# Performance work log

Hardware: AMD Instinct MI355X
Metric: run time of the kernel (lower is better)

## Reference

```python
import jax, jax.numpy as jnp
import numpy as np

B, H, S, D = 4, 16, 2048, 64
TEMPERATURE = 8.0  # sqrt(D)
NEG = -1000000000.0

def setup_inputs() -> dict:
    key = jax.random.key(0)
    kq, kk, kv, km = jax.random.split(key, 4)
    q = jax.random.normal(kq, (B, H, S, D), dtype=jnp.float32)
    k = jax.random.normal(kk, (B, H, S, D), dtype=jnp.float32)
    v = jax.random.normal(kv, (B, H, S, D), dtype=jnp.float32)
    mask = jax.random.randint(km, (B, 1, S, S), 0, 2, dtype=jnp.int32)
    return {"q": q, "k": k, "v": v, "mask": mask}

def reference(q, k, v, mask):
    # scores: [B,H,S,S]
    scores = jnp.einsum('bhqd,bhkd->bhqk', q / TEMPERATURE, k)
    scores = jnp.where(mask == 1, NEG, scores)
    attn = jax.nn.softmax(scores, axis=-1)  # dropout p=0.0 -> identity
    out = jnp.einsum('bhqk,bhkd->bhqd', attn, v)
    return out
```

## Files before the change

kernel.cpp:

```cpp
#include <hip/hip_runtime.h>

#define NB 4
#define NH 16
#define SS 2048
#define DD 64
#define QT 128
#define KT 64
#define LSP 72
#define QSCALE 0.18033688011112042f

#define MASK_BITS_BYTES ((size_t)NB * SS * (SS / 8))
#define KV_TILE_ELEMS   (KT * DD)
#define KV_BYTES        ((size_t)NB * NH * SS * DD * 2)
#define WS_NEED         (MASK_BITS_BYTES + 2 * KV_BYTES)

typedef __bf16 bf16x8 __attribute__((ext_vector_type(8)));
typedef __bf16 bf16x2 __attribute__((ext_vector_type(2)));
typedef float  floatx16 __attribute__((ext_vector_type(16)));

static_assert(sizeof(bf16x8) == 16, "bf16x8 must be 16B");

__device__ __forceinline__ int pack2(float a, float b) {
    bf16x2 v; v[0] = (__bf16)a; v[1] = (__bf16)b;
    return __builtin_bit_cast(int, v);
}

__global__ __launch_bounds__(256)
void pack_mask_kernel(const int* __restrict__ M, unsigned long long* __restrict__ bits)
{
    int gw   = (blockIdx.x * 256 + threadIdx.x) >> 6;
    int lane = threadIdx.x & 63;
    size_t row = (size_t)(gw >> 5);
    int word   = gw & 31;
    int mval = M[row * SS + (size_t)word * 64 + lane];
    unsigned long long b = __ballot(mval == 1);
    if (lane == 0) bits[gw] = b;
}

__global__ __launch_bounds__(256)
void convert_kv_kernel(const float* __restrict__ K, const float* __restrict__ V,
                       __bf16* __restrict__ Kt, __bf16* __restrict__ Vt)
{
    const int bh   = blockIdx.x >> 5;
    const int tile = blockIdx.x & 31;
    const int t    = threadIdx.x;
    const float* Kb = K + ((size_t)bh * SS + tile * KT) * DD;
    const float* Vb = V + ((size_t)bh * SS + tile * KT) * DD;
    __bf16* Ko = Kt + ((size_t)(bh * 32 + tile)) * KV_TILE_ELEMS;
    __bf16* Vo = Vt + ((size_t)(bh * 32 + tile)) * KV_TILE_ELEMS;

    {
        const int key = t >> 2, dg = (t & 3) * 16;
        const float* src = Kb + (size_t)key * DD + dg;
        __bf16 w[16];
        #pragma unroll
        for (int i = 0; i < 4; ++i) {
            float4 f = ((const float4*)src)[i];
            w[4*i+0] = (__bf16)f.x; w[4*i+1] = (__bf16)f.y;
            w[4*i+2] = (__bf16)f.z; w[4*i+3] = (__bf16)f.w;
        }
        *(uint4*)(Ko + (size_t)key * DD + dg)     = *(uint4*)&w[0];
        *(uint4*)(Ko + (size_t)key * DD + dg + 8) = *(uint4*)&w[8];
    }
    {
        const int dim = t >> 2, kg = (t & 3) * 16;
        __bf16 w[16];
        #pragma unroll
        for (int i = 0; i < 16; ++i) {
            int pos = (i & 3) + 8 * ((i >> 2) & 1) + 4 * ((i >> 3) & 1);
            w[pos] = (__bf16)Vb[(size_t)(kg + i) * DD + dim];
        }
        *(uint4*)(Vo + (size_t)dim * DD + kg)     = *(uint4*)&w[0];
        *(uint4*)(Vo + (size_t)dim * DD + kg + 8) = *(uint4*)&w[8];
    }
}

__global__ __launch_bounds__(256, 4)
void attn_kernel(const float* __restrict__ Q, const __bf16* __restrict__ Kt,
                 const __bf16* __restrict__ Vt, const uint2* __restrict__ MB,
                 float* __restrict__ O)
{
    __shared__ __bf16 ks[2][KT][LSP];
    __shared__ __bf16 vsT[2][DD][LSP];

    const int t    = threadIdx.x;
    const int wave = t >> 6;
    const int lane = t & 63;
    const int l31  = lane & 31;
    const int h8   = lane >> 5;

    const int bh    = blockIdx.x >> 4;
    const int qtile = blockIdx.x & 15;
    const int b     = bh >> 4;
    const int q0    = qtile * QT + wave * 32;

    const size_t base = (size_t)bh * SS * DD;
    const float*  Qb  = Q  + base;
    const __bf16* Ktb = Kt + base;
    const __bf16* Vtb = Vt + base;

    bf16x8 aq[4];
    {
        const float* qp = Qb + (size_t)(q0 + l31) * DD + 8 * h8;
        #pragma unroll
        for (int s = 0; s < 4; ++s) {
            float4 f0 = *(const float4*)(qp + 16 * s);
            float4 f1 = *(const float4*)(qp + 16 * s + 4);
            bf16x8 a;
            a[0] = (__bf16)(f0.x * QSCALE); a[1] = (__bf16)(f0.y * QSCALE);
            a[2] = (__bf16)(f0.z * QSCALE); a[3] = (__bf16)(f0.w * QSCALE);
            a[4] = (__bf16)(f1.x * QSCALE); a[5] = (__bf16)(f1.y * QSCALE);
            a[6] = (__bf16)(f1.z * QSCALE); a[7] = (__bf16)(f1.w * QSCALE);
            aq[s] = a;
        }
    }

    const int srow = t >> 2;
    const int scol = (t & 3) * 16;
    const __bf16* kp0 = Ktb + (size_t)srow * DD + scol;
    const __bf16* vp0 = Vtb + (size_t)srow * DD + scol;

    uint4 kr0 = ((const uint4*)kp0)[0], kr1 = ((const uint4*)(kp0 + 8))[0];
    uint4 vr0 = ((const uint4*)vp0)[0], vr1 = ((const uint4*)(vp0 + 8))[0];

    const uint2* mbrow = MB + ((size_t)b * SS + q0 + l31) * (SS / 64);
    uint2 mwc = mbrow[0];

    floatx16 o0, o1;
    #pragma unroll
    for (int i = 0; i < 16; ++i) { o0[i] = 0.f; o1[i] = 0.f; }
    float ls = 0.f;

    *(uint4*)&ks[0][srow][scol]      = kr0;
    *(uint4*)&ks[0][srow][scol + 8]  = kr1;
    *(uint4*)&vsT[0][srow][scol]     = vr0;
    *(uint4*)&vsT[0][srow][scol + 8] = vr1;

    {
        const __bf16* kn = kp0 + (size_t)KV_TILE_ELEMS;
        const __bf16* vn = vp0 + (size_t)KV_TILE_ELEMS;
        kr0 = ((const uint4*)kn)[0]; kr1 = ((const uint4*)(kn + 8))[0];
        vr0 = ((const uint4*)vn)[0]; vr1 = ((const uint4*)(vn + 8))[0];
    }

    for (int tt = 0; tt < SS / KT; ++tt) {
        __syncthreads();

        const int wb = (tt + 1) & 1;
        *(uint4*)&ks[wb][srow][scol]      = kr0;
        *(uint4*)&ks[wb][srow][scol + 8]  = kr1;
        *(uint4*)&vsT[wb][srow][scol]     = vr0;
        *(uint4*)&vsT[wb][srow][scol + 8] = vr1;

        uint2 mwn = mbrow[(tt + 1) & 31];
        {
            size_t off = (size_t)((tt + 2) & 31) * KV_TILE_ELEMS;
            const __bf16* kn = kp0 + off;
            const __bf16* vn = vp0 + off;
            kr0 = ((const uint4*)kn)[0]; kr1 = ((const uint4*)(kn + 8))[0];
            vr0 = ((const uint4*)vn)[0]; vr1 = ((const uint4*)(vn + 8))[0];
        }

        const __bf16 (*ksb)[LSP] = ks[tt & 1];
        const __bf16 (*vtb)[LSP] = vsT[tt & 1];

        #pragma unroll
        for (int h = 0; h < 2; ++h) {
            floatx16 c;
            #pragma unroll
            for (int i = 0; i < 16; ++i) c[i] = 0.f;
            #pragma unroll
            for (int s = 0; s < 4; ++s) {
                bf16x8 a = *(const bf16x8*)&ksb[32 * h + l31][16 * s + 8 * h8];
                c = __builtin_amdgcn_mfma_f32_32x32x16_bf16(a, aq[s], c, 0, 0, 0);
            }

            unsigned u = (h ? mwc.y : mwc.x) >> (4 * h8);
            int pk[8];
            float psum = 0.f;
            #pragma unroll
            for (int g = 0; g < 8; ++g) {
                const int ia = 2 * g, ib = 2 * g + 1;
                float pa = __builtin_amdgcn_exp2f(c[ia]);
                float pb = __builtin_amdgcn_exp2f(c[ib]);
                bool ma  = (u >> ((ia & 3) + 8 * (ia >> 2))) & 1;
                bool mb_ = (u >> ((ib & 3) + 8 * (ib >> 2))) & 1;
                pa = ma  ? 0.f : pa;
                pb = mb_ ? 0.f : pb;
                psum += pa + pb;
                pk[g] = pack2(pa, pb);
            }
            ls += psum;

            #pragma unroll
            for (int s2 = 0; s2 < 2; ++s2) {
                int4 fw; fw.x = pk[4*s2]; fw.y = pk[4*s2+1]; fw.z = pk[4*s2+2]; fw.w = pk[4*s2+3];
                bf16x8 bp = __builtin_bit_cast(bf16x8, fw);
                bf16x8 av0 = *(const bf16x8*)&vtb[l31][32 * h + 16 * s2 + 8 * h8];
                bf16x8 av1 = *(const bf16x8*)&vtb[32 + l31][32 * h + 16 * s2 + 8 * h8];
                o0 = __builtin_amdgcn_mfma_f32_32x32x16_bf16(av0, bp, o0, 0, 0, 0);
                o1 = __builtin_amdgcn_mfma_f32_32x32x16_bf16(av1, bp, o1, 0, 0, 0);
            }
        }
        mwc = mwn;
    }

    ls += __shfl_xor(ls, 32);
    float inv = 1.0f / ls;
    float* op = O + base + (size_t)(q0 + l31) * DD;
    #pragma unroll
    for (int s = 0; s < 4; ++s) {
        float4 st0, st1;
        st0.x = o0[4*s+0] * inv; st0.y = o0[4*s+1] * inv;
        st0.z = o0[4*s+2] * inv; st0.w = o0[4*s+3] * inv;
        st1.x = o1[4*s+0] * inv; st1.y = o1[4*s+1] * inv;
        st1.z = o1[4*s+2] * inv; st1.w = o1[4*s+3] * inv;
        *(float4*)(op + 8 * s + 4 * h8)      = st0;
        *(float4*)(op + 32 + 8 * s + 4 * h8) = st1;
    }
}

__global__ __launch_bounds__(256, 4)
void attn_kernel_fb(const float* __restrict__ Q, const float* __restrict__ K,
                    const float* __restrict__ V, const int* __restrict__ M,
                    float* __restrict__ O)
{
    __shared__ __bf16 ks[32][LSP];
    __shared__ __bf16 vsT[DD][40];

    const int t = threadIdx.x, wave = t >> 6, lane = t & 63;
    const int l31 = lane & 31, h8 = lane >> 5;
    const int bh = blockIdx.x >> 4, qtile = blockIdx.x & 15, b = bh >> 4;
    const int q0 = qtile * QT + wave * 32;
    const size_t base = (size_t)bh * SS * DD;
    const float* Qb = Q + base; const float* Kb = K + base; const float* Vb = V + base;

    bf16x8 aq[4];
    {
        const float* qp = Qb + (size_t)(q0 + l31) * DD + 8 * h8;
        #pragma unroll
        for (int s = 0; s < 4; ++s) {
            float4 f0 = *(const float4*)(qp + 16 * s);
            float4 f1 = *(const float4*)(qp + 16 * s + 4);
            bf16x8 a;
            a[0]=(__bf16)(f0.x*QSCALE); a[1]=(__bf16)(f0.y*QSCALE);
            a[2]=(__bf16)(f0.z*QSCALE); a[3]=(__bf16)(f0.w*QSCALE);
            a[4]=(__bf16)(f1.x*QSCALE); a[5]=(__bf16)(f1.y*QSCALE);
            a[6]=(__bf16)(f1.z*QSCALE); a[7]=(__bf16)(f1.w*QSCALE);
            aq[s] = a;
        }
    }
    const int skey = t >> 3, sdc = (t & 7) * 8;
    const int vk = 2 * (t & 15), vdc = (t >> 4) * 4;
    const int vcol = 16*(vk>>4) + 8*((vk>>2)&1) + (vk&3) + 4*((vk>>3)&1);
    const float* kp0 = Kb + (size_t)skey * DD + sdc;
    const float* vp0 = Vb + (size_t)vk * DD + vdc;
    float4 ka0 = ((const float4*)kp0)[0], ka1 = ((const float4*)kp0)[1];
    float4 va0 = *(const float4*)vp0, va1 = *(const float4*)(vp0 + DD);
    const int* mrow = M + (size_t)b * SS * SS + (size_t)(q0 + l31) * SS + 4 * h8;

    floatx16 o0, o1;
    #pragma unroll
    for (int i = 0; i < 16; ++i) { o0[i] = 0.f; o1[i] = 0.f; }
    float ls = 0.f;

    for (int tt = 0; tt < SS / 32; ++tt) {
        __syncthreads();
        {
            bf16x8 kw;
            kw[0]=(__bf16)ka0.x; kw[1]=(__bf16)ka0.y; kw[2]=(__bf16)ka0.z; kw[3]=(__bf16)ka0.w;
            kw[4]=(__bf16)ka1.x; kw[5]=(__bf16)ka1.y; kw[6]=(__bf16)ka1.z; kw[7]=(__bf16)ka1.w;
            *(bf16x8*)&ks[skey][sdc] = kw;
            float av[4] = {va0.x, va0.y, va0.z, va0.w};
            float bv[4] = {va1.x, va1.y, va1.z, va1.w};
            #pragma unroll
            for (int i = 0; i < 4; ++i) {
                bf16x2 pr; pr[0] = (__bf16)av[i]; pr[1] = (__bf16)bv[i];
                *(bf16x2*)&vsT[vdc + i][vcol] = pr;
            }
        }
        __syncthreads();
        int4 mi[4];
        #pragma unroll
        for (int g2 = 0; g2 < 4; ++g2) mi[g2] = *(const int4*)(mrow + tt * 32 + 8 * g2);
        {
            int jn = ((tt + 1) * 32) & (SS - 1);
            const float* kn = kp0 + (size_t)jn * DD;
            ka0 = ((const float4*)kn)[0]; ka1 = ((const float4*)kn)[1];
            const float* vn = vp0 + (size_t)jn * DD;
            va0 = *(const float4*)vn; va1 = *(const float4*)(vn + DD);
        }
        floatx16 c;
        #pragma unroll
        for (int i = 0; i < 16; ++i) c[i] = 0.f;
        #pragma unroll
        for (int s = 0; s < 4; ++s) {
            bf16x8 a = *(const bf16x8*)&ks[l31][16 * s + 8 * h8];
            c = __builtin_amdgcn_mfma_f32_32x32x16_bf16(a, aq[s], c, 0, 0, 0);
        }
        int pk[8]; float psum = 0.f;
        #pragma unroll
        for (int g = 0; g < 8; ++g) {
            const int ia = 2 * g, ib = 2 * g + 1;
            float pa = __builtin_amdgcn_exp2f(c[ia]);
            float pb = __builtin_amdgcn_exp2f(c[ib]);
            const int g2 = ia >> 2;
            pa = ((&mi[g2].x)[ia & 3] == 1) ? 0.f : pa;
            pb = ((&mi[g2].x)[ib & 3] == 1) ? 0.f : pb;
            psum += pa + pb;
            pk[g] = pack2(pa, pb);
        }
        ls += psum;
        #pragma unroll
        for (int s2 = 0; s2 < 2; ++s2) {
            int4 fw; fw.x = pk[4*s2]; fw.y = pk[4*s2+1]; fw.z = pk[4*s2+2]; fw.w = pk[4*s2+3];
            bf16x8 bp = __builtin_bit_cast(bf16x8, fw);
            bf16x8 av0 = *(const bf16x8*)&vsT[l31][16 * s2 + 8 * h8];
            bf16x8 av1 = *(const bf16x8*)&vsT[32 + l31][16 * s2 + 8 * h8];
            o0 = __builtin_amdgcn_mfma_f32_32x32x16_bf16(av0, bp, o0, 0, 0, 0);
            o1 = __builtin_amdgcn_mfma_f32_32x32x16_bf16(av1, bp, o1, 0, 0, 0);
        }
    }
    ls += __shfl_xor(ls, 32);
    float inv = 1.0f / ls;
    float* op = O + base + (size_t)(q0 + l31) * DD;
    #pragma unroll
    for (int s = 0; s < 4; ++s) {
        float4 st0, st1;
        st0.x=o0[4*s+0]*inv; st0.y=o0[4*s+1]*inv; st0.z=o0[4*s+2]*inv; st0.w=o0[4*s+3]*inv;
        st1.x=o1[4*s+0]*inv; st1.y=o1[4*s+1]*inv; st1.z=o1[4*s+2]*inv; st1.w=o1[4*s+3]*inv;
        *(float4*)(op + 8 * s + 4 * h8)      = st0;
        *(float4*)(op + 32 + 8 * s + 4 * h8) = st1;
    }
}

extern "C" void kernel_launch(void* const* d_in, const int* in_sizes, int n_in,
                              void* d_out, int out_size, void* d_ws, size_t ws_size,
                              hipStream_t stream) {
    (void)in_sizes; (void)n_in; (void)out_size;
    const float* q = (const float*)d_in[0];
    const float* k = (const float*)d_in[1];
    const float* v = (const float*)d_in[2];
    const int*   m = (const int*)d_in[3];
    float* out = (float*)d_out;
    dim3 grid(NB * NH * (SS / QT));

    if (ws_size >= WS_NEED) {
        unsigned long long* bits = (unsigned long long*)d_ws;
        __bf16* Kt = (__bf16*)((char*)d_ws + MASK_BITS_BYTES);
        __bf16* Vt = (__bf16*)((char*)d_ws + MASK_BITS_BYTES + KV_BYTES);
        pack_mask_kernel<<<dim3(NB * SS * (SS / 64) / 4), 256, 0, stream>>>(m, bits);
        convert_kv_kernel<<<dim3(NB * NH * 32), 256, 0, stream>>>(k, v, Kt, Vt);
        attn_kernel<<<grid, 256, 0, stream>>>(q, Kt, Vt, (const uint2*)bits, out);
    } else {
        attn_kernel_fb<<<grid, 256, 0, stream>>>(q, k, v, m, out);
    }
}
```

Before: 323.3 us.

## Process two 32-row query groups per wave to reuse K/V LDS fragments

Each wave now handles 64 query rows (two 32-row groups) instead of 32, so the query tile per block doubles to 256 and the grid halves. The K and V fragments loaded from LDS are reused across both query groups, which halves LDS reads and global K/V traffic per query row. In exchange, register pressure roughly doubles (two sets of accumulators and Q fragments), launch bounds drop to 2 blocks per CU, and there are only 512 blocks, which may reduce occupancy and latency hiding.

```diff
diff --git a/kernel.cpp b/kernel.cpp
--- a/kernel.cpp
+++ b/kernel.cpp
@@ -4,7 +4,7 @@
 #define NH 16
 #define SS 2048
 #define DD 64
-#define QT 128
+#define QT 256
 #define KT 64
 #define LSP 72
 #define QSCALE 0.18033688011112042f
@@ -75,7 +75,7 @@
     }
 }
 
-__global__ __launch_bounds__(256, 4)
+__global__ __launch_bounds__(256, 2)
 void attn_kernel(const float* __restrict__ Q, const __bf16* __restrict__ Kt,
                  const __bf16* __restrict__ Vt, const uint2* __restrict__ MB,
                  float* __restrict__ O)
@@ -89,19 +89,20 @@
     const int l31  = lane & 31;
     const int h8   = lane >> 5;
 
-    const int bh    = blockIdx.x >> 4;
-    const int qtile = blockIdx.x & 15;
+    const int bh    = blockIdx.x >> 3;
+    const int qtile = blockIdx.x & 7;
     const int b     = bh >> 4;
-    const int q0    = qtile * QT + wave * 32;
+    const int q0    = qtile * QT + wave * 64;
 
     const size_t base = (size_t)bh * SS * DD;
     const float*  Qb  = Q  + base;
     const __bf16* Ktb = Kt + base;
     const __bf16* Vtb = Vt + base;
 
-    bf16x8 aq[4];
-    {
-        const float* qp = Qb + (size_t)(q0 + l31) * DD + 8 * h8;
+    bf16x8 aq[2][4];
+    #pragma unroll
+    for (int qg = 0; qg < 2; ++qg) {
+        const float* qp = Qb + (size_t)(q0 + 32 * qg + l31) * DD + 8 * h8;
         #pragma unroll
         for (int s = 0; s < 4; ++s) {
             float4 f0 = *(const float4*)(qp + 16 * s);
@@ -111,7 +112,7 @@
             a[2] = (__bf16)(f0.z * QSCALE); a[3] = (__bf16)(f0.w * QSCALE);
             a[4] = (__bf16)(f1.x * QSCALE); a[5] = (__bf16)(f1.y * QSCALE);
             a[6] = (__bf16)(f1.z * QSCALE); a[7] = (__bf16)(f1.w * QSCALE);
-            aq[s] = a;
+            aq[qg][s] = a;
         }
     }
 
@@ -123,13 +124,18 @@
     uint4 kr0 = ((const uint4*)kp0)[0], kr1 = ((const uint4*)(kp0 + 8))[0];
     uint4 vr0 = ((const uint4*)vp0)[0], vr1 = ((const uint4*)(vp0 + 8))[0];
 
-    const uint2* mbrow = MB + ((size_t)b * SS + q0 + l31) * (SS / 64);
-    uint2 mwc = mbrow[0];
-
-    floatx16 o0, o1;
-    #pragma unroll
-    for (int i = 0; i < 16; ++i) { o0[i] = 0.f; o1[i] = 0.f; }
-    float ls = 0.f;
+    const uint2* mbrow0 = MB + ((size_t)b * SS + q0 + l31) * (SS / 64);
+    const uint2* mbrow1 = MB + ((size_t)b * SS + q0 + 32 + l31) * (SS / 64);
+    uint2 mwc[2] = {mbrow0[0], mbrow1[0]};
+
+    floatx16 o[2][2];
+    #pragma unroll
+    for (int qg = 0; qg < 2; ++qg)
+        #pragma unroll
+        for (int d = 0; d < 2; ++d)
+            #pragma unroll
+            for (int i = 0; i < 16; ++i) o[qg][d][i] = 0.f;
+    float ls[2] = {0.f, 0.f};
 
     *(uint4*)&ks[0][srow][scol]      = kr0;
     *(uint4*)&ks[0][srow][scol + 8]  = kr1;
@@ -152,7 +158,8 @@
         *(uint4*)&vsT[wb][srow][scol]     = vr0;
         *(uint4*)&vsT[wb][srow][scol + 8] = vr1;
 
-        uint2 mwn = mbrow[(tt + 1) & 31];
+        uint2 mwn0 = mbrow0[(tt + 1) & 31];
+        uint2 mwn1 = mbrow1[(tt + 1) & 31];
         {
             size_t off = (size_t)((tt + 2) & 31) * KV_TILE_ELEMS;
             const __bf16* kn = kp0 + off;
@@ -166,57 +173,73 @@
 
         #pragma unroll
         for (int h = 0; h < 2; ++h) {
-            floatx16 c;
-            #pragma unroll
-            for (int i = 0; i < 16; ++i) c[i] = 0.f;
-            #pragma unroll
-            for (int s = 0; s < 4; ++s) {
-                bf16x8 a = *(const bf16x8*)&ksb[32 * h + l31][16 * s + 8 * h8];
-                c = __builtin_amdgcn_mfma_f32_32x32x16_bf16(a, aq[s], c, 0, 0, 0);
+            bf16x8 a[4];
+            #pragma unroll
+            for (int s = 0; s < 4; ++s)
+                a[s] = *(const bf16x8*)&ksb[32 * h + l31][16 * s + 8 * h8];
+            bf16x8 av[4];
+            #pragma unroll
+            for (int s2 = 0; s2 < 2; ++s2) {
+                av[2*s2]   = *(const bf16x8*)&vtb[l31][32 * h + 16 * s2 + 8 * h8];
+                av[2*s2+1] = *(const bf16x8*)&vtb[32 + l31][32 * h + 16 * s2 + 8 * h8];
             }
 
-            unsigned u = (h ? mwc.y : mwc.x) >> (4 * h8);
-            int pk[8];
-            float psum = 0.f;
-            #pragma unroll
-            for (int g = 0; g < 8; ++g) {
-                const int ia = 2 * g, ib = 2 * g + 1;
-                float pa = __builtin_amdgcn_exp2f(c[ia]);
-                float pb = __builtin_amdgcn_exp2f(c[ib]);
-                bool ma  = (u >> ((ia & 3) + 8 * (ia >> 2))) & 1;
-                bool mb_ = (u >> ((ib & 3) + 8 * (ib >> 2))) & 1;
-                pa = ma  ? 0.f : pa;
-                pb = mb_ ? 0.f : pb;
-                psum += pa + pb;
-                pk[g] = pack2(pa, pb);
+            #pragma unroll
+            for (int qg = 0; qg < 2; ++qg) {
+                floatx16 c;
+                #pragma unroll
+                for (int i = 0; i < 16; ++i) c[i] = 0.f;
+                #pragma unroll
+                for (int s = 0; s < 4; ++s)
+                    c = __builtin_amdgcn_mfma_f32_32x32x16_bf16(a[s], aq[qg][s], c, 0, 0, 0);
+
+                const uint2 mv = qg ? mwc[1] : mwc[0];
+                unsigned u = (h ? mv.y : mv.x) >> (4 * h8);
+                int pk[8];
+                float psum = 0.f;
+                #pragma unroll
+                for (int g = 0; g < 8; ++g) {
+                    const int ia = 2 * g, ib = 2 * g + 1;
+                    float pa = __builtin_amdgcn_exp2f(c[ia]);
+                    float pb = __builtin_amdgcn_exp2f(c[ib]);
+                    bool ma  = (u >> ((ia & 3) + 8 * (ia >> 2))) & 1;
+                    bool mb_ = (u >> ((ib & 3) + 8 * (ib >> 2))) & 1;
+                    pa = ma  ? 0.f : pa;
+                    pb = mb_ ? 0.f : pb;
+                    psum += pa + pb;
+                    pk[g] = pack2(pa, pb);
+                }
+                ls[qg] += psum;
+
+                #pragma unroll
+                for (int s2 = 0; s2 < 2; ++s2) {
+                    int4 fw; fw.x = pk[4*s2]; fw.y = pk[4*s2+1]; fw.z = pk[4*s2+2]; fw.w = pk[4*s2+3];
+                    bf16x8 bp = __builtin_bit_cast(bf16x8, fw);
+                    o[qg][0] = __builtin_amdgcn_mfma_f32_32x32x16_bf16(av[2*s2],   bp, o[qg][0], 0, 0, 0);
+                    o[qg][1] = __builtin_amdgcn_mfma_f32_32x32x16_bf16(av[2*s2+1], bp, o[qg][1], 0, 0, 0);
+                }
             }
-            ls += psum;
-
-            #pragma unroll
-            for (int s2 = 0; s2 < 2; ++s2) {
-                int4 fw; fw.x = pk[4*s2]; fw.y = pk[4*s2+1]; fw.z = pk[4*s2+2]; fw.w = pk[4*s2+3];
-                bf16x8 bp = __builtin_bit_cast(bf16x8, fw);
-                bf16x8 av0 = *(const bf16x8*)&vtb[l31][32 * h + 16 * s2 + 8 * h8];
-                bf16x8 av1 = *(const bf16x8*)&vtb[32 + l31][32 * h + 16 * s2 + 8 * h8];
-                o0 = __builtin_amdgcn_mfma_f32_32x32x16_bf16(av0, bp, o0, 0, 0, 0);
-                o1 = __builtin_amdgcn_mfma_f32_32x32x16_bf16(av1, bp, o1, 0, 0, 0);
-            }
-        }
-        mwc = mwn;
-    }
-
-    ls += __shfl_xor(ls, 32);
-    float inv = 1.0f / ls;
-    float* op = O + base + (size_t)(q0 + l31) * DD;
-    #pragma unroll
-    for (int s = 0; s < 4; ++s) {
-        float4 st0, st1;
-        st0.x = o0[4*s+0] * inv; st0.y = o0[4*s+1] * inv;
-        st0.z = o0[4*s+2] * inv; st0.w = o0[4*s+3] * inv;
-        st1.x = o1[4*s+0] * inv; st1.y = o1[4*s+1] * inv;
-        st1.z = o1[4*s+2] * inv; st1.w = o1[4*s+3] * inv;
-        *(float4*)(op + 8 * s + 4 * h8)      = st0;
-        *(float4*)(op + 32 + 8 * s + 4 * h8) = st1;
+        }
+        mwc[0] = mwn0;
+        mwc[1] = mwn1;
+    }
+
+    #pragma unroll
+    for (int qg = 0; qg < 2; ++qg) {
+        float l = ls[qg];
+        l += __shfl_xor(l, 32);
+        float inv = 1.0f / l;
+        float* op = O + base + (size_t)(q0 + 32 * qg + l31) * DD;
+        #pragma unroll
+        for (int s = 0; s < 4; ++s) {
+            float4 st0, st1;
+            st0.x = o[qg][0][4*s+0] * inv; st0.y = o[qg][0][4*s+1] * inv;
+            st0.z = o[qg][0][4*s+2] * inv; st0.w = o[qg][0][4*s+3] * inv;
+            st1.x = o[qg][1][4*s+0] * inv; st1.y = o[qg][1][4*s+1] * inv;
+            st1.z = o[qg][1][4*s+2] * inv; st1.w = o[qg][1][4*s+3] * inv;
+            *(float4*)(op + 8 * s + 4 * h8)      = st0;
+            *(float4*)(op + 32 + 8 * s + 4 * h8) = st1;
+        }
     }
 }
 
@@ -231,7 +254,7 @@
     const int t = threadIdx.x, wave = t >> 6, lane = t & 63;
     const int l31 = lane & 31, h8 = lane >> 5;
     const int bh = blockIdx.x >> 4, qtile = blockIdx.x & 15, b = bh >> 4;
-    const int q0 = qtile * QT + wave * 32;
+    const int q0 = qtile * 128 + wave * 32;
     const size_t base = (size_t)bh * SS * DD;
     const float* Qb = Q + base; const float* Kb = K + base; const float* Vb = V + base;
 
@@ -343,7 +366,6 @@
     const float* v = (const float*)d_in[2];
     const int*   m = (const int*)d_in[3];
     float* out = (float*)d_out;
-    dim3 grid(NB * NH * (SS / QT));
 
     if (ws_size >= WS_NEED) {
         unsigned long long* bits = (unsigned long long*)d_ws;
@@ -351,8 +373,8 @@
         __bf16* Vt = (__bf16*)((char*)d_ws + MASK_BITS_BYTES + KV_BYTES);
         pack_mask_kernel<<<dim3(NB * SS * (SS / 64) / 4), 256, 0, stream>>>(m, bits);
         convert_kv_kernel<<<dim3(NB * NH * 32), 256, 0, stream>>>(k, v, Kt, Vt);
-        attn_kernel<<<grid, 256, 0, stream>>>(q, Kt, Vt, (const uint2*)bits, out);
+        attn_kernel<<<dim3(NB * NH * (SS / QT)), 256, 0, stream>>>(q, Kt, Vt, (const uint2*)bits, out);
     } else {
-        attn_kernel_fb<<<grid, 256, 0, stream>>>(q, k, v, m, out);
-    }
-}
+        attn_kernel_fb<<<dim3(NB * NH * 16), 256, 0, stream>>>(q, k, v, m, out);
+    }
+}
```

Result: no change. 328.2 us (+1.5%).

## Pre-swizzle K/V into MFMA fragment layout and read directly from global

Applied to the files above, without the earlier changes.

The K/V conversion kernel now writes bf16 tiles in the exact per-lane fragment order the MFMA operands need. The attention kernel then loads operands straight from global memory (L2-cached) and drops the LDS double buffer and the per-tile __syncthreads. Alternate waves process the two key halves in opposite order to spread load traffic. This removes LDS staging and barrier cost, but every wave now re-reads K/V from cache and the explicit one-tile-ahead prefetch is gone, so load latency may be exposed.

```diff
diff --git a/kernel.cpp b/kernel.cpp
--- a/kernel.cpp
+++ b/kernel.cpp
@@ -6,7 +6,6 @@
 #define DD 64
 #define QT 128
 #define KT 64
-#define LSP 72
 #define QSCALE 0.18033688011112042f
 
 #define MASK_BITS_BYTES ((size_t)NB * SS * (SS / 8))
@@ -50,8 +49,9 @@
     __bf16* Vo = Vt + ((size_t)(bh * 32 + tile)) * KV_TILE_ELEMS;
 
     {
-        const int key = t >> 2, dg = (t & 3) * 16;
-        const float* src = Kb + (size_t)key * DD + dg;
+        const int key = t >> 2, dg16 = t & 3;
+        const int h = key >> 5, l31 = key & 31;
+        const float* src = Kb + (size_t)key * DD + dg16 * 16;
         __bf16 w[16];
         #pragma unroll
         for (int i = 0; i < 4; ++i) {
@@ -59,19 +59,24 @@
             w[4*i+0] = (__bf16)f.x; w[4*i+1] = (__bf16)f.y;
             w[4*i+2] = (__bf16)f.z; w[4*i+3] = (__bf16)f.w;
         }
-        *(uint4*)(Ko + (size_t)key * DD + dg)     = *(uint4*)&w[0];
-        *(uint4*)(Ko + (size_t)key * DD + dg + 8) = *(uint4*)&w[8];
+        __bf16* dst = Ko + (size_t)(h * 4 + dg16) * 512;
+        *(uint4*)(dst + (size_t)l31 * 8)        = *(uint4*)&w[0];
+        *(uint4*)(dst + (size_t)(32 + l31) * 8) = *(uint4*)&w[8];
     }
     {
-        const int dim = t >> 2, kg = (t & 3) * 16;
+        const int dim = t >> 2, kg16 = t & 3;
+        const int kg = kg16 * 16;
+        const int d = dim >> 5, l31 = dim & 31;
+        const int h = kg >> 5, s2 = (kg >> 4) & 1;
         __bf16 w[16];
         #pragma unroll
         for (int i = 0; i < 16; ++i) {
             int pos = (i & 3) + 8 * ((i >> 2) & 1) + 4 * ((i >> 3) & 1);
             w[pos] = (__bf16)Vb[(size_t)(kg + i) * DD + dim];
         }
-        *(uint4*)(Vo + (size_t)dim * DD + kg)     = *(uint4*)&w[0];
-        *(uint4*)(Vo + (size_t)dim * DD + kg + 8) = *(uint4*)&w[8];
+        __bf16* dst = Vo + (size_t)(h * 4 + s2 * 2 + d) * 512;
+        *(uint4*)(dst + (size_t)l31 * 8)        = *(uint4*)&w[0];
+        *(uint4*)(dst + (size_t)(32 + l31) * 8) = *(uint4*)&w[8];
     }
 }
 
@@ -80,9 +85,6 @@
                  const __bf16* __restrict__ Vt, const uint2* __restrict__ MB,
                  float* __restrict__ O)
 {
-    __shared__ __bf16 ks[2][KT][LSP];
-    __shared__ __bf16 vsT[2][DD][LSP];
-
     const int t    = threadIdx.x;
     const int wave = t >> 6;
     const int lane = t & 63;
@@ -95,9 +97,7 @@
     const int q0    = qtile * QT + wave * 32;
 
     const size_t base = (size_t)bh * SS * DD;
-    const float*  Qb  = Q  + base;
-    const __bf16* Ktb = Kt + base;
-    const __bf16* Vtb = Vt + base;
+    const float*  Qb  = Q + base;
 
     bf16x8 aq[4];
     {
@@ -115,13 +115,8 @@
         }
     }
 
-    const int srow = t >> 2;
-    const int scol = (t & 3) * 16;
-    const __bf16* kp0 = Ktb + (size_t)srow * DD + scol;
-    const __bf16* vp0 = Vtb + (size_t)srow * DD + scol;
-
-    uint4 kr0 = ((const uint4*)kp0)[0], kr1 = ((const uint4*)(kp0 + 8))[0];
-    uint4 vr0 = ((const uint4*)vp0)[0], vr1 = ((const uint4*)(vp0 + 8))[0];
+    const __bf16* kt = Kt + base + (size_t)lane * 8;
+    const __bf16* vt = Vt + base + (size_t)lane * 8;
 
     const uint2* mbrow = MB + ((size_t)b * SS + q0 + l31) * (SS / 64);
     uint2 mwc = mbrow[0];
@@ -131,49 +126,31 @@
     for (int i = 0; i < 16; ++i) { o0[i] = 0.f; o1[i] = 0.f; }
     float ls = 0.f;
 
-    *(uint4*)&ks[0][srow][scol]      = kr0;
-    *(uint4*)&ks[0][srow][scol + 8]  = kr1;
-    *(uint4*)&vsT[0][srow][scol]     = vr0;
-    *(uint4*)&vsT[0][srow][scol + 8] = vr1;
-
-    {
-        const __bf16* kn = kp0 + (size_t)KV_TILE_ELEMS;
-        const __bf16* vn = vp0 + (size_t)KV_TILE_ELEMS;
-        kr0 = ((const uint4*)kn)[0]; kr1 = ((const uint4*)(kn + 8))[0];
-        vr0 = ((const uint4*)vn)[0]; vr1 = ((const uint4*)(vn + 8))[0];
-    }
+    const int wpar = wave & 1;
 
     for (int tt = 0; tt < SS / KT; ++tt) {
-        __syncthreads();
-
-        const int wb = (tt + 1) & 1;
-        *(uint4*)&ks[wb][srow][scol]      = kr0;
-        *(uint4*)&ks[wb][srow][scol + 8]  = kr1;
-        *(uint4*)&vsT[wb][srow][scol]     = vr0;
-        *(uint4*)&vsT[wb][srow][scol + 8] = vr1;
-
+        const __bf16* ktt = kt + (size_t)tt * KV_TILE_ELEMS;
+        const __bf16* vtt = vt + (size_t)tt * KV_TILE_ELEMS;
         uint2 mwn = mbrow[(tt + 1) & 31];
-        {
-            size_t off = (size_t)((tt + 2) & 31) * KV_TILE_ELEMS;
-            const __bf16* kn = kp0 + off;
-            const __bf16* vn = vp0 + off;
-            kr0 = ((const uint4*)kn)[0]; kr1 = ((const uint4*)(kn + 8))[0];
-            vr0 = ((const uint4*)vn)[0]; vr1 = ((const uint4*)(vn + 8))[0];
-        }
-
-        const __bf16 (*ksb)[LSP] = ks[tt & 1];
-        const __bf16 (*vtb)[LSP] = vsT[tt & 1];
-
-        #pragma unroll
-        for (int h = 0; h < 2; ++h) {
+
+        #pragma unroll
+        for (int hh = 0; hh < 2; ++hh) {
+            const int h = hh ^ wpar;
+
+            bf16x8 a[4], av[4];
+            #pragma unroll
+            for (int s = 0; s < 4; ++s)
+                a[s] = *(const bf16x8*)(ktt + (size_t)(h * 4 + s) * 512);
+            #pragma unroll
+            for (int i = 0; i < 4; ++i)
+                av[i] = *(const bf16x8*)(vtt + (size_t)(h * 4 + i) * 512);
+
             floatx16 c;
             #pragma unroll
             for (int i = 0; i < 16; ++i) c[i] = 0.f;
             #pragma unroll
-            for (int s = 0; s < 4; ++s) {
-                bf16x8 a = *(const bf16x8*)&ksb[32 * h + l31][16 * s + 8 * h8];
-                c = __builtin_amdgcn_mfma_f32_32x32x16_bf16(a, aq[s], c, 0, 0, 0);
-            }
+            for (int s = 0; s < 4; ++s)
+                c = __builtin_amdgcn_mfma_f32_32x32x16_bf16(a[s], aq[s], c, 0, 0, 0);
 
             unsigned u = (h ? mwc.y : mwc.x) >> (4 * h8);
             int pk[8];
@@ -196,10 +173,8 @@
             for (int s2 = 0; s2 < 2; ++s2) {
                 int4 fw; fw.x = pk[4*s2]; fw.y = pk[4*s2+1]; fw.z = pk[4*s2+2]; fw.w = pk[4*s2+3];
                 bf16x8 bp = __builtin_bit_cast(bf16x8, fw);
-                bf16x8 av0 = *(const bf16x8*)&vtb[l31][32 * h + 16 * s2 + 8 * h8];
-                bf16x8 av1 = *(const bf16x8*)&vtb[32 + l31][32 * h + 16 * s2 + 8 * h8];
-                o0 = __builtin_amdgcn_mfma_f32_32x32x16_bf16(av0, bp, o0, 0, 0, 0);
-                o1 = __builtin_amdgcn_mfma_f32_32x32x16_bf16(av1, bp, o1, 0, 0, 0);
+                o0 = __builtin_amdgcn_mfma_f32_32x32x16_bf16(av[2*s2],   bp, o0, 0, 0, 0);
+                o1 = __builtin_amdgcn_mfma_f32_32x32x16_bf16(av[2*s2+1], bp, o1, 0, 0, 0);
             }
         }
         mwc = mwn;
@@ -225,13 +200,13 @@
                     const float* __restrict__ V, const int* __restrict__ M,
                     float* __restrict__ O)
 {
-    __shared__ __bf16 ks[32][LSP];
+    __shared__ __bf16 ks[32][72];
     __shared__ __bf16 vsT[DD][40];
 
     const int t = threadIdx.x, wave = t >> 6, lane = t & 63;
     const int l31 = lane & 31, h8 = lane >> 5;
     const int bh = blockIdx.x >> 4, qtile = blockIdx.x & 15, b = bh >> 4;
-    const int q0 = qtile * QT + wave * 32;
+    const int q0 = qtile * 128 + wave * 32;
     const size_t base = (size_t)bh * SS * DD;
     const float* Qb = Q + base; const float* Kb = K + base; const float* Vb = V + base;
 
@@ -343,7 +318,6 @@
     const float* v = (const float*)d_in[2];
     const int*   m = (const int*)d_in[3];
     float* out = (float*)d_out;
-    dim3 grid(NB * NH * (SS / QT));
 
     if (ws_size >= WS_NEED) {
         unsigned long long* bits = (unsigned long long*)d_ws;
@@ -351,8 +325,8 @@
         __bf16* Vt = (__bf16*)((char*)d_ws + MASK_BITS_BYTES + KV_BYTES);
         pack_mask_kernel<<<dim3(NB * SS * (SS / 64) / 4), 256, 0, stream>>>(m, bits);
         convert_kv_kernel<<<dim3(NB * NH * 32), 256, 0, stream>>>(k, v, Kt, Vt);
-        attn_kernel<<<grid, 256, 0, stream>>>(q, Kt, Vt, (const uint2*)bits, out);
+        attn_kernel<<<dim3(NB * NH * (SS / QT)), 256, 0, stream>>>(q, Kt, Vt, (const uint2*)bits, out);
     } else {
-        attn_kernel_fb<<<grid, 256, 0, stream>>>(q, k, v, m, out);
-    }
-}
+        attn_kernel_fb<<<dim3(NB * NH * 16), 256, 0, stream>>>(q, k, v, m, out);
+    }
+}
```

Result: faster. 310.8 us (-3.8%).
